# Kernel optimization log

Measured on AMD Instinct MI355X. Metric: run time of the kernel, lower is better.

The kernel has to match this reference:

```python
import jax, jax.numpy as jnp
import numpy as np

N_CHANNEL = 64
N_BAND = 5
N_CLASS = 2
B = 64
K = 2 * N_CHANNEL  # nodes covered by the fully-connected edge_index


def _w(key, shape):
    fan_in = shape[0] if len(shape) == 2 else int(np.prod(shape[1:]))
    return (jax.random.normal(key, shape, jnp.float32) / np.float32(np.sqrt(fan_in)))


def setup_inputs() -> dict:
    key = jax.random.key(0)
    ks = jax.random.split(key, 22)
    d = {}
    d['x1'] = jax.random.normal(ks[0], (B, K, N_BAND), jnp.float32)
    d['x2'] = jax.random.normal(ks[1], (B, K, K), jnp.float32)
    # GCNConv params (weights stored (in, out); PyG applies linear then aggregates, bias after)
    d['gcn1_w'] = _w(ks[2], (N_BAND, 2 * N_BAND))
    d['gcn1_b'] = 0.01 * jax.random.normal(ks[3], (2 * N_BAND,), jnp.float32)
    d['gcn2_w'] = _w(ks[4], (2 * N_BAND, 1))
    d['gcn2_b'] = 0.01 * jax.random.normal(ks[5], (1,), jnp.float32)
    d['fcg_w'] = _w(ks[6], (K, K))
    d['fcg_b'] = 0.01 * jax.random.normal(ks[7], (K,), jnp.float32)
    d['conv1_w'] = _w(ks[8], (16, 1, 3, 3))   # OIHW
    d['conv1_b'] = 0.01 * jax.random.normal(ks[9], (16,), jnp.float32)
    d['conv2_w'] = _w(ks[10], (16, 16, 3, 3))
    d['conv2_b'] = 0.01 * jax.random.normal(ks[11], (16,), jnp.float32)
    d['fcc_w'] = _w(ks[12], (16 * K * K, K))
    d['fcc_b'] = 0.01 * jax.random.normal(ks[13], (K,), jnp.float32)
    d['fc1_w'] = _w(ks[14], (4 * N_CHANNEL, 2 * N_CHANNEL))
    d['fc1_b'] = 0.01 * jax.random.normal(ks[15], (2 * N_CHANNEL,), jnp.float32)
    d['fc2_w'] = _w(ks[16], (2 * N_CHANNEL, N_CHANNEL))
    d['fc2_b'] = 0.01 * jax.random.normal(ks[17], (N_CHANNEL,), jnp.float32)
    d['fc3_w'] = _w(ks[18], (N_CHANNEL, N_CLASS))
    d['fc3_b'] = 0.01 * jax.random.normal(ks[19], (N_CLASS,), jnp.float32)
    return d


def _gcn(x, W, b):
    # Faithful to original: edge_index is fully connected over the FIRST K rows only.
    # With default self-loops, normalized adjacency over rows [0,K) is (1/K)*ones(K,K)
    # (all degrees = K); every other row has only its self-loop (degree 1 -> identity).
    y = x @ W                                   # (B*N, out)
    y = y.at[:K].set(jnp.mean(y[:K], axis=0))   # broadcast mean over first K rows
    return y + b


def _conv(x, w, b):
    y = jax.lax.conv_general_dilated(x, w, (1, 1), 'SAME',
                                     dimension_numbers=('NCHW', 'OIHW', 'NCHW'))
    return jax.nn.relu(y + b[None, :, None, None])


def reference(x1, x2, gcn1_w, gcn1_b, gcn2_w, gcn2_b, fcg_w, fcg_b,
              conv1_w, conv1_b, conv2_w, conv2_b, fcc_w, fcc_b,
              fc1_w, fc1_b, fc2_w, fc2_b, fc3_w, fc3_b):
    Bn, N, Feat = x1.shape
    # GNN branch (dropout is identity in eval mode)
    h = x1.reshape(Bn * N, Feat)
    h = jax.nn.relu(_gcn(h, gcn1_w, gcn1_b))
    h = jax.nn.relu(_gcn(h, gcn2_w, gcn2_b))
    h = h.reshape(Bn, -1)                       # (B, 2*n_channel)
    g = jax.nn.relu(h @ fcg_w + fcg_b)
    # CNN branch
    c = x2[:, None]                             # (B,1,H,W)
    c = _conv(c, conv1_w, conv1_b)
    c = _conv(c, conv2_w, conv2_b)
    c = c.reshape(Bn, -1)                       # channel-major flatten, same as torch .view
    c = jax.nn.relu(c @ fcc_w + fcc_b)
    # Fusion MLP
    x = jnp.concatenate([c, g], axis=1)
    x = jax.nn.relu(x @ fc1_w + fc1_b)
    x = jax.nn.relu(x @ fc2_w + fc2_b)
    return jax.nn.sigmoid(x @ fc3_w + fc3_b)
```

## Files before the change

kernel.cpp:

```cpp
#include <hip/hip_runtime.h>
#include <hip/hip_bf16.h>


#define NROWS   8192
#define IMG     16384
#define FCC_K   262144
#define FCC_BLOCKS 512
#define FCC_KRANGE 512
#define FCC_CHUNK 128

typedef __attribute__((ext_vector_type(8))) short bf16x8;
typedef __attribute__((ext_vector_type(4))) float f32x4;
typedef __attribute__((ext_vector_type(4))) unsigned short us4;
typedef __attribute__((ext_vector_type(8))) unsigned short us8;

__device__ __forceinline__ unsigned short f2bf(float f) {
    unsigned u = __float_as_uint(f);
    unsigned r = (u + 0x7FFFu + ((u >> 16) & 1u)) >> 16;
    return (unsigned short)r;
}

__global__ __launch_bounds__(128) void gcnfcg_kernel(
    const float* __restrict__ x1,
    const float* __restrict__ W1,
    const float* __restrict__ b1,
    const float* __restrict__ W2,
    const float* __restrict__ b2,
    const float* __restrict__ fcgW,
    const float* __restrict__ fcgb,
    float* __restrict__ g)
{
    __shared__ float sW1[50], sb1[10], sW2[10], smean[10];
    __shared__ float sy1[128][10];
    __shared__ float sh2[128];
    int b = blockIdx.x, t = threadIdx.x;
    if (t < 50) sW1[t] = W1[t];
    if (t < 10) { sb1[t] = b1[t]; sW2[t] = W2[t]; }
    __syncthreads();

    int r = b*128 + t;
    float x[5];
    #pragma unroll
    for (int f = 0; f < 5; ++f) x[f] = x1[r*5 + f];
    float y[10];
    #pragma unroll
    for (int o = 0; o < 10; ++o) {
        float a = 0.f;
        #pragma unroll
        for (int f = 0; f < 5; ++f) a += x[f] * sW1[f*10 + o];
        y[o] = a;
    }

    float h1row[10];
    if (b == 0) {
        #pragma unroll
        for (int o = 0; o < 10; ++o) sy1[t][o] = y[o];
        __syncthreads();
        if (t < 10) {
            float s = 0.f;
            for (int rr = 0; rr < 128; ++rr) s += sy1[rr][t];
            smean[t] = fmaxf(s * (1.f/128.f) + sb1[t], 0.f);
        }
        __syncthreads();
        #pragma unroll
        for (int o = 0; o < 10; ++o) h1row[o] = smean[o];
    } else {
        #pragma unroll
        for (int o = 0; o < 10; ++o) h1row[o] = fmaxf(y[o] + sb1[o], 0.f);
    }

    float y2 = 0.f;
    #pragma unroll
    for (int o = 0; o < 10; ++o) y2 += h1row[o] * sW2[o];
    sh2[t] = fmaxf(y2 + b2[0], 0.f);
    __syncthreads();

    float acc = fcgb[t];
    #pragma unroll 8
    for (int k = 0; k < 128; ++k) acc += sh2[k] * fcgW[k*128 + t];
    g[b*128 + t] = fmaxf(acc, 0.f);
}

__global__ __launch_bounds__(256) void conv12_kernel(
    const float* __restrict__ x2,
    const float* __restrict__ w1,
    const float* __restrict__ b1,
    const float* __restrict__ w2,
    const float* __restrict__ b2,
    unsigned short* __restrict__ c2bf)
{
    __shared__ float sx2[8][130];
    __shared__ unsigned short sin[6*130*16];
    __shared__ unsigned short sB[5*512];
    __shared__ float sw1[144], sb1v[16];

    int tid = threadIdx.x;
    int blk = blockIdx.x;
    int b   = blk >> 5;
    int R0  = (blk & 31) * 4;

    if (tid < 144) sw1[tid] = w1[tid];
    if (tid < 16)  sb1v[tid] = b1[tid];

    for (int idx = tid; idx < 2560; idx += 256) {
        int q   = idx >> 9;
        int rem = idx & 511;
        int l   = rem >> 3;
        int e   = rem & 7;
        int k   = (l >> 4) * 8 + e;
        int oc  = l & 15;
        int ic  = k & 15;
        int dd  = 2*q + (k >> 4);
        unsigned short bits = 0;
        if (dd < 9) bits = f2bf(w2[oc*144 + ic*9 + dd]);
        sB[idx] = bits;
    }
    if (tid < 192) {
        int rr = tid >> 5, rem = tid & 31;
        int cc = (rem < 16) ? 0 : 129;
        sin[(rr*130 + cc)*16 + (rem & 15)] = 0;
    }
    {
        const float* xb = x2 + (size_t)b * IMG;
        for (int idx = tid; idx < 8*130; idx += 256) {
            int rr = idx / 130, cc = idx - rr*130;
            int ri = R0 - 2 + rr, gj = cc - 1;
            float v = 0.f;
            if (ri >= 0 && ri < 128 && gj >= 0 && gj < 128)
                v = xb[ri*128 + gj];
            sx2[rr][cc] = v;
        }
    }
    __syncthreads();

    for (int p = tid; p < 768; p += 256) {
        int rr = p >> 7;
        int cc = p & 127;
        int ri1 = R0 - 1 + rr;
        bool valid = (ri1 >= 0 && ri1 < 128);
        float in9[3][3];
        #pragma unroll
        for (int di = 0; di < 3; ++di)
          #pragma unroll
          for (int dj = 0; dj < 3; ++dj)
              in9[di][dj] = sx2[rr + di][cc + dj];
        us8 o0, o1;
        #pragma unroll
        for (int oc = 0; oc < 16; ++oc) {
            float acc = sb1v[oc];
            #pragma unroll
            for (int di = 0; di < 3; ++di)
              #pragma unroll
              for (int dj = 0; dj < 3; ++dj)
                  acc += in9[di][dj] * sw1[oc*9 + di*3 + dj];
            unsigned short bits = valid ? f2bf(fmaxf(acc, 0.f)) : (unsigned short)0;
            if (oc < 8) o0[oc] = bits; else o1[oc - 8] = bits;
        }
        unsigned short* dst = &sin[(rr*130 + cc + 1)*16];
        *reinterpret_cast<us8*>(dst)     = o0;
        *reinterpret_cast<us8*>(dst + 8) = o1;
    }
    __syncthreads();

    int lane = tid & 63;
    int wv   = tid >> 6;
    int ln   = lane & 15;
    int g    = lane >> 4;
    int ghalf = g & 1;

    int aoff[5];
    #pragma unroll
    for (int q = 0; q < 5; ++q) {
        int dd = 2*q + (g >> 1);
        if (dd > 8) dd = 8;
        int di = dd / 3, dj = dd % 3;
        aoff[q] = ((wv + di)*130 + ln + dj)*16 + ghalf*8;
    }

    bf16x8 bf[5];
    #pragma unroll
    for (int q = 0; q < 5; ++q)
        bf[q] = *reinterpret_cast<const bf16x8*>(&sB[q*512 + lane*8]);

    float bias_oc = b2[ln];
    int r = R0 + wv;
    unsigned short* outbase = c2bf + ((size_t)b*16 + ln)*IMG + r*128;

    #pragma unroll
    for (int t = 0; t < 8; ++t) {
        f32x4 acc = {0.f, 0.f, 0.f, 0.f};
        #pragma unroll
        for (int q = 0; q < 5; ++q) {
            bf16x8 a = *reinterpret_cast<const bf16x8*>(&sin[aoff[q] + t*256]);
            acc = __builtin_amdgcn_mfma_f32_16x16x32_bf16(a, bf[q], acc, 0, 0, 0);
        }
        int pc = t*16 + g*4;
        #pragma unroll
        for (int reg = 0; reg < 4; ++reg)
            outbase[pc + reg] = f2bf(fmaxf(acc[reg] + bias_oc, 0.f));
    }
}

__global__ __launch_bounds__(256, 3) void fcc_mfma(
    const unsigned short* __restrict__ c2bf,
    const float* __restrict__ W,
    float* __restrict__ partials)
{
    __shared__ unsigned short sWt[128*128];

    int tid  = threadIdx.x;
    int blk  = blockIdx.x;
    int k0   = blk * FCC_KRANGE;
    int lane = tid & 63, wv = tid >> 6;
    int ln   = lane & 15, g = lane >> 4;

    int q  = tid & 31;
    int kO = tid >> 5;

    f32x4 acc[8];
    #pragma unroll
    for (int j = 0; j < 8; ++j) acc[j] = (f32x4){0.f,0.f,0.f,0.f};

    const float* Wb = W + (size_t)k0 * 128;
    const unsigned short* arow = c2bf + (size_t)(16*wv + ln)*FCC_K + k0 + g*8;

    for (int ci = 0; ci < 4; ++ci) {
        const float* Wc = Wb + (size_t)ci * FCC_CHUNK * 128;
        #pragma unroll
        for (int ko2 = 0; ko2 < 2; ++ko2) {
            int kbase = ko2*64 + kO*8;
            float4 rows[8];
            #pragma unroll
            for (int r = 0; r < 8; ++r)
                rows[r] = *reinterpret_cast<const float4*>(
                    Wc + (size_t)(kbase + r)*128 + q*4);
            us8 vc0, vc1, vc2, vc3;
            #pragma unroll
            for (int r = 0; r < 8; ++r) {
                vc0[r] = f2bf(rows[r].x);
                vc1[r] = f2bf(rows[r].y);
                vc2[r] = f2bf(rows[r].z);
                vc3[r] = f2bf(rows[r].w);
            }
            int col0 = q*4;
            *reinterpret_cast<us8*>(&sWt[((col0+0)*128 + kbase) ^ (((col0+0)&7)<<3)]) = vc0;
            *reinterpret_cast<us8*>(&sWt[((col0+1)*128 + kbase) ^ (((col0+1)&7)<<3)]) = vc1;
            *reinterpret_cast<us8*>(&sWt[((col0+2)*128 + kbase) ^ (((col0+2)&7)<<3)]) = vc2;
            *reinterpret_cast<us8*>(&sWt[((col0+3)*128 + kbase) ^ (((col0+3)&7)<<3)]) = vc3;
        }
        __syncthreads();

        bf16x8 af[4];
        #pragma unroll
        for (int ks = 0; ks < 4; ++ks)
            af[ks] = *reinterpret_cast<const bf16x8*>(arow + ci*FCC_CHUNK + ks*32);

        #pragma unroll
        for (int ks = 0; ks < 4; ++ks) {
            #pragma unroll
            for (int j = 0; j < 8; ++j) {
                int col = j*16 + ln;
                int idx = (col*128 + ks*32 + g*8) ^ ((col&7)<<3);
                bf16x8 bfrag = *reinterpret_cast<const bf16x8*>(&sWt[idx]);
                acc[j] = __builtin_amdgcn_mfma_f32_16x16x32_bf16(af[ks], bfrag, acc[j], 0, 0, 0);
            }
        }
        __syncthreads();
    }

    float* p = partials + (size_t)blk * 8192;
    #pragma unroll
    for (int j = 0; j < 8; ++j)
      #pragma unroll
      for (int reg = 0; reg < 4; ++reg) {
          int m = 16*wv + g*4 + reg;
          p[m*128 + j*16 + ln] = acc[j][reg];
      }
}

__global__ __launch_bounds__(128) void head_kernel(
    const float* __restrict__ partials,
    const float* __restrict__ fccb,
    const float* __restrict__ g,
    const float* __restrict__ w1, const float* __restrict__ bb1,
    const float* __restrict__ w2, const float* __restrict__ bb2,
    const float* __restrict__ w3, const float* __restrict__ bb3,
    float* __restrict__ out)
{
    __shared__ float sx[256], sh[128], s2[64];
    int b = blockIdx.x, tid = threadIdx.x;

    const float* pb = partials + (size_t)b*128 + tid;
    float s = 0.f;
    #pragma unroll 8
    for (int p = 0; p < FCC_BLOCKS; ++p) s += pb[(size_t)p*8192];
    sx[tid]       = fmaxf(s + fccb[tid], 0.f);
    sx[128 + tid] = g[b*128 + tid];
    __syncthreads();
    {
        float acc = bb1[tid];
        for (int k = 0; k < 256; ++k) acc += sx[k] * w1[k*128 + tid];
        sh[tid] = fmaxf(acc, 0.f);
    }
    __syncthreads();
    if (tid < 64) {
        float acc = bb2[tid];
        for (int k = 0; k < 128; ++k) acc += sh[k] * w2[k*64 + tid];
        s2[tid] = fmaxf(acc, 0.f);
    }
    __syncthreads();
    if (tid < 2) {
        float acc = bb3[tid];
        for (int k = 0; k < 64; ++k) acc += s2[k] * w3[k*2 + tid];
        out[b*2 + tid] = 1.f / (1.f + __expf(-acc));
    }
}

extern "C" void kernel_launch(void* const* d_in, const int* in_sizes, int n_in,
                              void* d_out, int out_size, void* d_ws, size_t ws_size,
                              hipStream_t stream)
{
    const float* x1      = (const float*)d_in[0];
    const float* x2      = (const float*)d_in[1];
    const float* gcn1_w  = (const float*)d_in[2];
    const float* gcn1_b  = (const float*)d_in[3];
    const float* gcn2_w  = (const float*)d_in[4];
    const float* gcn2_b  = (const float*)d_in[5];
    const float* fcg_w   = (const float*)d_in[6];
    const float* fcg_b   = (const float*)d_in[7];
    const float* conv1_w = (const float*)d_in[8];
    const float* conv1_b = (const float*)d_in[9];
    const float* conv2_w = (const float*)d_in[10];
    const float* conv2_b = (const float*)d_in[11];
    const float* fcc_w   = (const float*)d_in[12];
    const float* fcc_b   = (const float*)d_in[13];
    const float* fc1_w   = (const float*)d_in[14];
    const float* fc1_b   = (const float*)d_in[15];
    const float* fc2_w   = (const float*)d_in[16];
    const float* fc2_b   = (const float*)d_in[17];
    const float* fc3_w   = (const float*)d_in[18];
    const float* fc3_b   = (const float*)d_in[19];
    float* out = (float*)d_out;

    float* ws = (float*)d_ws;
    float* g        = ws;
    unsigned short* c2bf = (unsigned short*)(g + 8192);
    float* partials = (float*)(c2bf + 16777216);

    gcnfcg_kernel<<<64, 128, 0, stream>>>(x1, gcn1_w, gcn1_b, gcn2_w, gcn2_b,
                                          fcg_w, fcg_b, g);
    conv12_kernel<<<2048, 256, 0, stream>>>(x2, conv1_w, conv1_b,
                                            conv2_w, conv2_b, c2bf);
    fcc_mfma<<<FCC_BLOCKS, 256, 0, stream>>>(c2bf, fcc_w, partials);
    head_kernel<<<64, 128, 0, stream>>>(partials, fcc_b, g, fc1_w, fc1_b,
                                        fc2_w, fc2_b, fc3_w, fc3_b, out);
}
```

Before: 110.3 us.

## Widen LDS swizzle, vectorize conv output stores, parallelize head partial reduction

Changes the fcc weight-tile XOR swizzle to mix more column bits, aiming to cut LDS bank conflicts on the transposed bf16 writes and fragment reads. Packs the four bf16 conv outputs per lane into a single 8-byte store instead of four scalar stores. Makes the head kernel use 512 threads, so four groups each reduce a quarter of the 512 fcc partials and then combine through shared memory, shortening the serial reduction. Each is a separate local tweak; the swizzle must stay consistent between the write and read sides.

```diff
diff --git a/kernel.cpp b/kernel.cpp
--- a/kernel.cpp
+++ b/kernel.cpp
@@ -18,6 +18,10 @@
     unsigned u = __float_as_uint(f);
     unsigned r = (u + 0x7FFFu + ((u >> 16) & 1u)) >> 16;
     return (unsigned short)r;
+}
+
+__device__ __forceinline__ int fcc_swz(int col, int k) {
+    return col*128 + (k ^ ((((col >> 2) ^ col) & 15) << 3));
 }
 
 __global__ __launch_bounds__(128) void gcnfcg_kernel(
@@ -195,9 +199,11 @@
             acc = __builtin_amdgcn_mfma_f32_16x16x32_bf16(a, bf[q], acc, 0, 0, 0);
         }
         int pc = t*16 + g*4;
+        us4 pk;
         #pragma unroll
         for (int reg = 0; reg < 4; ++reg)
-            outbase[pc + reg] = f2bf(fmaxf(acc[reg] + bias_oc, 0.f));
+            pk[reg] = f2bf(fmaxf(acc[reg] + bias_oc, 0.f));
+        *reinterpret_cast<us4*>(&outbase[pc]) = pk;
     }
 }
 
@@ -243,10 +249,10 @@
                 vc3[r] = f2bf(rows[r].w);
             }
             int col0 = q*4;
-            *reinterpret_cast<us8*>(&sWt[((col0+0)*128 + kbase) ^ (((col0+0)&7)<<3)]) = vc0;
-            *reinterpret_cast<us8*>(&sWt[((col0+1)*128 + kbase) ^ (((col0+1)&7)<<3)]) = vc1;
-            *reinterpret_cast<us8*>(&sWt[((col0+2)*128 + kbase) ^ (((col0+2)&7)<<3)]) = vc2;
-            *reinterpret_cast<us8*>(&sWt[((col0+3)*128 + kbase) ^ (((col0+3)&7)<<3)]) = vc3;
+            *reinterpret_cast<us8*>(&sWt[fcc_swz(col0+0, kbase)]) = vc0;
+            *reinterpret_cast<us8*>(&sWt[fcc_swz(col0+1, kbase)]) = vc1;
+            *reinterpret_cast<us8*>(&sWt[fcc_swz(col0+2, kbase)]) = vc2;
+            *reinterpret_cast<us8*>(&sWt[fcc_swz(col0+3, kbase)]) = vc3;
         }
         __syncthreads();
 
@@ -260,8 +266,8 @@
             #pragma unroll
             for (int j = 0; j < 8; ++j) {
                 int col = j*16 + ln;
-                int idx = (col*128 + ks*32 + g*8) ^ ((col&7)<<3);
-                bf16x8 bfrag = *reinterpret_cast<const bf16x8*>(&sWt[idx]);
+                bf16x8 bfrag = *reinterpret_cast<const bf16x8*>(
+                    &sWt[fcc_swz(col, ks*32 + g*8)]);
                 acc[j] = __builtin_amdgcn_mfma_f32_16x16x32_bf16(af[ks], bfrag, acc[j], 0, 0, 0);
             }
         }
@@ -278,7 +284,7 @@
       }
 }
 
-__global__ __launch_bounds__(128) void head_kernel(
+__global__ __launch_bounds__(512) void head_kernel(
     const float* __restrict__ partials,
     const float* __restrict__ fccb,
     const float* __restrict__ g,
@@ -287,32 +293,42 @@
     const float* __restrict__ w3, const float* __restrict__ bb3,
     float* __restrict__ out)
 {
+    __shared__ float sred[4][128];
     __shared__ float sx[256], sh[128], s2[64];
-    int b = blockIdx.x, tid = threadIdx.x;
-
-    const float* pb = partials + (size_t)b*128 + tid;
+    int b = blockIdx.x, t = threadIdx.x;
+    int o = t & 127, pr = t >> 7;
+
+    const float* pb = partials + (size_t)pr*8192 + (size_t)b*128 + o;
     float s = 0.f;
     #pragma unroll 8
-    for (int p = 0; p < FCC_BLOCKS; ++p) s += pb[(size_t)p*8192];
-    sx[tid]       = fmaxf(s + fccb[tid], 0.f);
-    sx[128 + tid] = g[b*128 + tid];
-    __syncthreads();
-    {
-        float acc = bb1[tid];
-        for (int k = 0; k < 256; ++k) acc += sx[k] * w1[k*128 + tid];
-        sh[tid] = fmaxf(acc, 0.f);
-    }
-    __syncthreads();
-    if (tid < 64) {
-        float acc = bb2[tid];
-        for (int k = 0; k < 128; ++k) acc += sh[k] * w2[k*64 + tid];
-        s2[tid] = fmaxf(acc, 0.f);
-    }
-    __syncthreads();
-    if (tid < 2) {
-        float acc = bb3[tid];
-        for (int k = 0; k < 64; ++k) acc += s2[k] * w3[k*2 + tid];
-        out[b*2 + tid] = 1.f / (1.f + __expf(-acc));
+    for (int p = 0; p < FCC_BLOCKS/4; ++p) s += pb[(size_t)p*4*8192];
+    sred[pr][o] = s;
+    __syncthreads();
+
+    if (t < 128) {
+        sx[t] = fmaxf(sred[0][t] + sred[1][t] + sred[2][t] + sred[3][t]
+                      + fccb[t], 0.f);
+    } else if (t < 256) {
+        sx[t] = g[b*128 + (t - 128)];
+    }
+    __syncthreads();
+
+    if (t < 128) {
+        float acc = bb1[t];
+        for (int k = 0; k < 256; ++k) acc += sx[k] * w1[k*128 + t];
+        sh[t] = fmaxf(acc, 0.f);
+    }
+    __syncthreads();
+    if (t < 64) {
+        float acc = bb2[t];
+        for (int k = 0; k < 128; ++k) acc += sh[k] * w2[k*64 + t];
+        s2[t] = fmaxf(acc, 0.f);
+    }
+    __syncthreads();
+    if (t < 2) {
+        float acc = bb3[t];
+        for (int k = 0; k < 64; ++k) acc += s2[k] * w3[k*2 + t];
+        out[b*2 + t] = 1.f / (1.f + __expf(-acc));
     }
 }
 
@@ -352,6 +368,6 @@
     conv12_kernel<<<2048, 256, 0, stream>>>(x2, conv1_w, conv1_b,
                                             conv2_w, conv2_b, c2bf);
     fcc_mfma<<<FCC_BLOCKS, 256, 0, stream>>>(c2bf, fcc_w, partials);
-    head_kernel<<<64, 128, 0, stream>>>(partials, fcc_b, g, fc1_w, fc1_b,
+    head_kernel<<<64, 512, 0, stream>>>(partials, fcc_b, g, fc1_w, fc1_b,
                                         fc2_w, fc2_b, fc3_w, fc3_b, out);
 }
```

Result: faster. 96.22 us (-12.8%).
